# Kernel optimization log

Measured on AMD Instinct MI355X. Metric: run time of the kernel, lower is better.

Reference implementation:

```python
import jax, jax.numpy as jnp
import numpy as np

B, S, D, H = 16, 784, 768, 12
DH = D // H  # 64


def rotate_half(x):
    # (x1, x2, x3, x4) -> (-x2, x1, -x4, x3), interleaved
    x_even = x[..., ::2]
    x_odd = x[..., 1::2]
    return jnp.stack((-x_odd, x_even), axis=-1).reshape(x.shape)


def setup_inputs() -> dict:
    key = jax.random.key(0)
    ks = jax.random.split(key, 12)
    s = 0.02
    return {
        "hidden_states": jax.random.normal(ks[0], (B, S, D), jnp.float32),
        "rotary_pos_emb": jax.random.uniform(ks[1], (B, S, DH), jnp.float32) * 6.28,
        "wq": jax.random.normal(ks[2], (D, D), jnp.float32) * s,
        "bq": jax.random.normal(ks[3], (D,), jnp.float32) * s,
        "wk": jax.random.normal(ks[4], (D, D), jnp.float32) * s,
        "bk": jax.random.normal(ks[5], (D,), jnp.float32) * s,
        "wv": jax.random.normal(ks[6], (D, D), jnp.float32) * s,
        "bv": jax.random.normal(ks[7], (D,), jnp.float32) * s,
        "wo": jax.random.normal(ks[8], (D, D), jnp.float32) * s,
        "bo": jax.random.normal(ks[9], (D,), jnp.float32) * s,
    }


def reference(hidden_states, rotary_pos_emb, wq, bq, wk, bk, wv, bv, wo, bo):
    scale = DH ** -0.5
    # Linear: x @ W^T + b; reshape to [B, H, S, DH]
    def proj(w, b):
        y = jnp.einsum("bsd,ed->bse", hidden_states, w) + b
        return y.reshape(B, S, H, DH).transpose(0, 2, 1, 3)

    q = proj(wq, bq)
    k = proj(wk, bk)
    v = proj(wv, bv)

    # RoPE: freqs [B, S, DH] -> [B, 1, S, DH] broadcast over heads
    cos = jnp.cos(rotary_pos_emb)[:, None, :, :]
    sin = jnp.sin(rotary_pos_emb)[:, None, :, :]
    q = q * cos + rotate_half(q) * sin
    k = k * cos + rotate_half(k) * sin

    attn = jnp.einsum("bhqd,bhkd->bhqk", q, k) * scale
    attn = jax.nn.softmax(attn, axis=-1)
    out = jnp.einsum("bhqk,bhkd->bhqd", attn, v)
    out = out.transpose(0, 2, 1, 3).reshape(B, S, D)
    out = jnp.einsum("bsd,ed->bse", out, wo) + bo
    return out
```

## Files before the change

kernel.cpp:

```cpp
#include <hip/hip_runtime.h>
#include <cstdint>
#include <cstddef>

constexpr int kB  = 16;
constexpr int kS  = 784;
constexpr int kD  = 768;
constexpr int kH  = 12;
constexpr int kM  = kB * kS;
constexpr int kSP = 832;

typedef __attribute__((ext_vector_type(8))) short bf16x8;
typedef __attribute__((ext_vector_type(4))) float floatx4;

__device__ __forceinline__ unsigned short f2bf(float x) {
    union { float f; unsigned int u; } v; v.f = x;
    unsigned int r = v.u + 0x7fffu + ((v.u >> 16) & 1u);
    return (unsigned short)(r >> 16);
}
__device__ __forceinline__ float bf2f(unsigned short h) {
    union { unsigned int u; float f; } v; v.u = ((unsigned int)h) << 16;
    return v.f;
}

__device__ __forceinline__ void gload_lds16(const void* g, void* l) {
    __builtin_amdgcn_global_load_lds(
        (const __attribute__((address_space(1))) void*)g,
        (__attribute__((address_space(3))) void*)l,
        16, 0, 0);
}

constexpr int kHsF4   = (kM * kD) / 4;
constexpr int kWF4    = (kD * kD) / 4;
constexpr int kPreTot = kHsF4 + 4 * kWF4 + (kM * 64) / 4;

__global__ __launch_bounds__(256)
void convert_pre(const float* __restrict__ hs, const float* __restrict__ rot,
                 const float* __restrict__ wq, const float* __restrict__ wk,
                 const float* __restrict__ wv, const float* __restrict__ wo,
                 const float* __restrict__ bq, const float* __restrict__ bk,
                 const float* __restrict__ bv,
                 unsigned short* __restrict__ hsB, unsigned short* __restrict__ wB,
                 unsigned int* __restrict__ csT, float* __restrict__ biasC)
{
    const int i = blockIdx.x * 256 + threadIdx.x;
    if (i < kHsF4) {
        float4 v = ((const float4*)hs)[i];
        ushort4 o = { f2bf(v.x), f2bf(v.y), f2bf(v.z), f2bf(v.w) };
        ((ushort4*)hsB)[i] = o;
    } else if (i < kHsF4 + 4 * kWF4) {
        const int j = i - kHsF4;
        const int w = j / kWF4, jj = j - w * kWF4;
        const float* src = (w == 0) ? wq : (w == 1) ? wk : (w == 2) ? wv : wo;
        float4 v = ((const float4*)src)[jj];
        ushort4 o = { f2bf(v.x), f2bf(v.y), f2bf(v.z), f2bf(v.w) };
        ((ushort4*)(wB + (size_t)w * (kD * kD)))[jj] = o;
    } else if (i < kPreTot) {
        const int j = i - kHsF4 - 4 * kWF4;
        float4 v = ((const float4*)rot)[j];
        float a[4] = { v.x, v.y, v.z, v.w };
        #pragma unroll
        for (int e = 0; e < 4; ++e) {
            float s, c;
            __sincosf(a[e], &s, &c);
            csT[j * 4 + e] = (unsigned)f2bf(c) | ((unsigned)f2bf(s) << 16);
        }
    } else {
        const int j = i - kPreTot;
        if (j < 3 * kD)
            biasC[j] = (j < kD) ? bq[j] : (j < 2 * kD) ? bk[j - kD] : bv[j - 2 * kD];
    }
}

enum { MODE_QKV = 0, MODE_OUT = 1 };

template<int MODE>
__global__ __launch_bounds__(256, 2)
void gemm_k(const unsigned short* __restrict__ A, const unsigned short* __restrict__ W,
            const float* __restrict__ bias, const unsigned int* __restrict__ csT,
            unsigned short* __restrict__ Qp, unsigned short* __restrict__ Kp,
            unsigned short* __restrict__ Vtp, float* __restrict__ Op)
{
    constexpr int BN  = (MODE == MODE_QKV) ? 256 : 128;
    constexpr int NTL = (MODE == MODE_QKV) ? 9 : 6;
    constexpr int NTC = BN / 32;
    constexpr int WJ  = BN / 64;

    __shared__ unsigned short As[2][4096];
    __shared__ unsigned short Ws[2][BN * 32];

    const int lin   = blockIdx.x;
    const int group = lin / (8 * NTL);
    const int rem   = lin - group * (8 * NTL);
    const int base_m = group * 8;
    int m_tile, n_tile;
    if (base_m + 8 <= 98) { m_tile = base_m + (rem & 7); n_tile = rem >> 3; }
    else                  { m_tile = base_m + (rem & 1); n_tile = rem >> 1; }
    const int m0 = m_tile * 128;
    const int n0 = n_tile * BN;

    const int tid  = threadIdx.x;
    const int wave = tid >> 6;
    const int lane = tid & 63;
    const int quad = lane >> 4;
    const int l16  = lane & 15;
    const int wm = wave >> 1, wn = wave & 1;

    floatx4 acc[4][NTC];
    #pragma unroll
    for (int mt = 0; mt < 4; ++mt)
        #pragma unroll
        for (int nt = 0; nt < NTC; ++nt)
            acc[mt][nt] = {0.f, 0.f, 0.f, 0.f};

    const int sidx0 = wave * 128 + lane;
    const int srow0 = sidx0 >> 2, sseg0 = (sidx0 & 3) ^ ((srow0 >> 1) & 3);
    const int sidx1 = sidx0 + 64;
    const int srow1 = sidx1 >> 2, sseg1 = (sidx1 & 3) ^ ((srow1 >> 1) & 3);
    int wrow[WJ], wseg[WJ];
    #pragma unroll
    for (int j = 0; j < WJ; ++j) {
        const int cid = wave * BN + j * 64 + lane;
        wrow[j] = cid >> 2;
        wseg[j] = (cid & 3) ^ ((wrow[j] >> 1) & 3);
    }

    gload_lds16(A + (size_t)(m0 + srow0) * kD + sseg0 * 8, &As[0][wave * 1024]);
    gload_lds16(A + (size_t)(m0 + srow1) * kD + sseg1 * 8, &As[0][wave * 1024 + 512]);
    #pragma unroll
    for (int j = 0; j < WJ; ++j)
        gload_lds16(W + (size_t)(n0 + wrow[j]) * kD + wseg[j] * 8,
                    &Ws[0][(wave * BN + j * 64) * 8]);

    for (int ks = 0; ks < 24; ++ks) {
        __syncthreads();
        if (ks < 23) {
            const int nb = (ks + 1) & 1;
            const int k0 = (ks + 1) * 32;
            gload_lds16(A + (size_t)(m0 + srow0) * kD + k0 + sseg0 * 8, &As[nb][wave * 1024]);
            gload_lds16(A + (size_t)(m0 + srow1) * kD + k0 + sseg1 * 8, &As[nb][wave * 1024 + 512]);
            #pragma unroll
            for (int j = 0; j < WJ; ++j)
                gload_lds16(W + (size_t)(n0 + wrow[j]) * kD + k0 + wseg[j] * 8,
                            &Ws[nb][(wave * BN + j * 64) * 8]);
        }
        const unsigned short* as_ = As[ks & 1];
        const unsigned short* ws_ = Ws[ks & 1];

        bf16x8 af[4], bw[NTC];
        #pragma unroll
        for (int mt = 0; mt < 4; ++mt) {
            const int row = wm * 64 + mt * 16 + l16;
            const int slot = quad ^ ((row >> 1) & 3);
            af[mt] = *(const bf16x8*)&as_[row * 32 + slot * 8];
        }
        #pragma unroll
        for (int nt = 0; nt < NTC; ++nt) {
            const int row = wn * (BN / 2) + nt * 16 + l16;
            const int slot = quad ^ ((row >> 1) & 3);
            bw[nt] = *(const bf16x8*)&ws_[row * 32 + slot * 8];
        }
        #pragma unroll
        for (int mt = 0; mt < 4; ++mt)
            #pragma unroll
            for (int nt = 0; nt < NTC; ++nt)
                acc[mt][nt] = __builtin_amdgcn_mfma_f32_16x16x32_bf16(
                    af[mt], bw[nt], acc[mt][nt], 0, 0, 0);
    }

    if constexpr (MODE == MODE_OUT) {
        #pragma unroll
        for (int nt = 0; nt < NTC; ++nt) {
            const int n = n0 + wn * (BN / 2) + nt * 16 + l16;
            const float bv = bias[n];
            #pragma unroll
            for (int mt = 0; mt < 4; ++mt)
                #pragma unroll
                for (int r = 0; r < 4; ++r) {
                    const int m = m0 + wm * 64 + mt * 16 + quad * 4 + r;
                    Op[(size_t)m * kD + n] = acc[mt][nt][r] + bv;
                }
        }
    } else {
        const int proj = n_tile / 3;
        if (proj < 2) {
            unsigned short* dst = proj ? Kp : Qp;
            const float scale = proj ? 1.0f : 0.125f;
            #pragma unroll
            for (int nt = 0; nt < NTC; ++nt) {
                const int n = n0 + wn * (BN / 2) + nt * 16 + l16;
                const float bv = bias[n];
                const int col = n - proj * kD;
                const int dh = col & 63;
                const int odd = l16 & 1;
                #pragma unroll
                for (int mt = 0; mt < 4; ++mt)
                    #pragma unroll
                    for (int r = 0; r < 4; ++r) {
                        const int m = m0 + wm * 64 + mt * 16 + quad * 4 + r;
                        const float val = acc[mt][nt][r] + bv;
                        const float px = __shfl_xor(val, 1);
                        const unsigned u = csT[(size_t)m * 64 + dh];
                        const float c = bf2f((unsigned short)(u & 0xffffu));
                        const float s = bf2f((unsigned short)(u >> 16));
                        const float out = odd ? (val * c + px * s) : (val * c - px * s);
                        dst[(size_t)m * kD + col] = f2bf(out * scale);
                    }
            }
        } else {
            #pragma unroll
            for (int nt = 0; nt < NTC; ++nt) {
                const int n = n0 + wn * (BN / 2) + nt * 16 + l16;
                const float bv = bias[n];
                const int col = n - 2 * kD;
                const int h = col >> 6, dh = col & 63;
                #pragma unroll
                for (int mt = 0; mt < 4; ++mt) {
                    const int m_r0 = m0 + wm * 64 + mt * 16 + quad * 4;
                    const int b = m_r0 / kS;
                    const int s = m_r0 - b * kS;
                    ushort4 pk;
                    pk.x = f2bf(acc[mt][nt][0] + bv);
                    pk.y = f2bf(acc[mt][nt][1] + bv);
                    pk.z = f2bf(acc[mt][nt][2] + bv);
                    pk.w = f2bf(acc[mt][nt][3] + bv);
                    *(ushort4*)(Vtp + (size_t)((b * kH + h) * 64 + dh) * kSP + s) = pk;
                }
            }
        }
    }
}

__global__ __launch_bounds__(256)
void flash_attn(const unsigned short* __restrict__ Qg,
                const unsigned short* __restrict__ Kg,
                const unsigned short* __restrict__ Vtg,
                unsigned short* __restrict__ Og)
{
    __shared__ unsigned short KV[2][8192];
    __shared__ unsigned short Ps[4][32 * 68];

    const int lin   = blockIdx.x;
    const int group = lin / 56;
    const int rem   = lin - group * 56;
    const int bh = group * 8 + (rem & 7);
    const int qt = rem >> 3;
    const int b = bh / kH, h = bh - b * kH;
    const int tid = threadIdx.x, wave = tid >> 6, lane = tid & 63;
    const int quad = lane >> 4, l16 = lane & 15;
    const int q0 = qt * 128;
    const size_t rowBase = (size_t)(b * kS) * kD + h * 64;

    #pragma unroll
    for (int j = 0; j < 4; ++j) {
        const int idx = (wave * 4 + j) * 64 + lane;
        const int row = idx >> 3, slot = idx & 7, seg = slot ^ (row & 7);
        gload_lds16(Qg + rowBase + (size_t)(q0 + row) * kD + seg * 8,
                    &KV[0][(wave * 4 + j) * 512]);
    }
    __syncthreads();
    bf16x8 aq[2][2];
    #pragma unroll
    for (int mt = 0; mt < 2; ++mt)
        #pragma unroll
        for (int ch = 0; ch < 2; ++ch) {
            const int row = wave * 32 + mt * 16 + l16;
            const int slot = (ch * 4 + quad) ^ (row & 7);
            aq[mt][ch] = *(const bf16x8*)&KV[0][row * 64 + slot * 8];
        }
    __syncthreads();

    const int cidx0 = wave * 128 + lane;
    const int crow0 = cidx0 >> 3, cseg0 = (cidx0 & 7) ^ (crow0 & 7);
    const int cidx1 = cidx0 + 64;
    const int crow1 = cidx1 >> 3, cseg1 = (cidx1 & 7) ^ (crow1 & 7);

    {
        gload_lds16(Kg + rowBase + (size_t)(crow0)*kD + cseg0 * 8, &KV[0][wave * 1024]);
        gload_lds16(Vtg + (size_t)(bh * 64 + crow0) * kSP + cseg0 * 8, &KV[0][4096 + wave * 1024]);
        gload_lds16(Kg + rowBase + (size_t)(crow1)*kD + cseg1 * 8, &KV[0][wave * 1024 + 512]);
        gload_lds16(Vtg + (size_t)(bh * 64 + crow1) * kSP + cseg1 * 8, &KV[0][4096 + wave * 1024 + 512]);
    }

    floatx4 oacc[2][4];
    #pragma unroll
    for (int mt = 0; mt < 2; ++mt)
        #pragma unroll
        for (int nt = 0; nt < 4; ++nt)
            oacc[mt][nt] = {0.f, 0.f, 0.f, 0.f};
    float lrow[2][4];
    #pragma unroll
    for (int mt = 0; mt < 2; ++mt)
        #pragma unroll
        for (int r = 0; r < 4; ++r) lrow[mt][r] = 0.f;

    for (int kt = 0; kt < 13; ++kt) {
        __syncthreads();
        if (kt < 12) {
            const int nb = (kt + 1) & 1;
            const int kr = (kt + 1) * 64;
            gload_lds16(Kg + rowBase + (size_t)(kr + crow0) * kD + cseg0 * 8,
                        &KV[nb][wave * 1024]);
            gload_lds16(Vtg + (size_t)(bh * 64 + crow0) * kSP + kr + cseg0 * 8,
                        &KV[nb][4096 + wave * 1024]);
            gload_lds16(Kg + rowBase + (size_t)(kr + crow1) * kD + cseg1 * 8,
                        &KV[nb][wave * 1024 + 512]);
            gload_lds16(Vtg + (size_t)(bh * 64 + crow1) * kSP + kr + cseg1 * 8,
                        &KV[nb][4096 + wave * 1024 + 512]);
        }
        const unsigned short* Ks = &KV[kt & 1][0];
        const unsigned short* Vs = &KV[kt & 1][4096];

        bf16x8 bk[4][2];
        #pragma unroll
        for (int nt = 0; nt < 4; ++nt)
            #pragma unroll
            for (int ch = 0; ch < 2; ++ch) {
                const int row = nt * 16 + l16;
                const int slot = (ch * 4 + quad) ^ (row & 7);
                bk[nt][ch] = *(const bf16x8*)&Ks[row * 64 + slot * 8];
            }

        floatx4 sc[2][4];
        #pragma unroll
        for (int mt = 0; mt < 2; ++mt)
            #pragma unroll
            for (int nt = 0; nt < 4; ++nt) {
                sc[mt][nt] = {0.f, 0.f, 0.f, 0.f};
                sc[mt][nt] = __builtin_amdgcn_mfma_f32_16x16x32_bf16(
                    aq[mt][0], bk[nt][0], sc[mt][nt], 0, 0, 0);
                sc[mt][nt] = __builtin_amdgcn_mfma_f32_16x16x32_bf16(
                    aq[mt][1], bk[nt][1], sc[mt][nt], 0, 0, 0);
            }

        if (kt == 12) {
            #pragma unroll
            for (int mt = 0; mt < 2; ++mt)
                #pragma unroll
                for (int nt = 1; nt < 4; ++nt)
                    #pragma unroll
                    for (int r = 0; r < 4; ++r) sc[mt][nt][r] = -1e30f;
        }

        #pragma unroll
        for (int mt = 0; mt < 2; ++mt)
            #pragma unroll
            for (int nt = 0; nt < 4; ++nt)
                #pragma unroll
                for (int r = 0; r < 4; ++r) {
                    const float p = __expf(sc[mt][nt][r]);
                    union { float f; unsigned u; } pu; pu.f = p;
                    union { unsigned u; float f; } pt; pt.u = pu.u & 0xFFFF0000u;
                    lrow[mt][r] += pt.f;
                    Ps[wave][(mt * 16 + quad * 4 + r) * 68 + nt * 16 + l16] =
                        (unsigned short)(pu.u >> 16);
                }

        bf16x8 ap[2][2];
        #pragma unroll
        for (int mt = 0; mt < 2; ++mt)
            #pragma unroll
            for (int ks = 0; ks < 2; ++ks)
                ap[mt][ks] = *(const bf16x8*)&Ps[wave][(mt * 16 + l16) * 68 + ks * 32 + quad * 8];

        #pragma unroll
        for (int ks = 0; ks < 2; ++ks)
            #pragma unroll
            for (int nt = 0; nt < 4; ++nt) {
                const int row = nt * 16 + l16;
                const int slot = (ks * 4 + quad) ^ (row & 7);
                const bf16x8 bv = *(const bf16x8*)&Vs[row * 64 + slot * 8];
                #pragma unroll
                for (int mt = 0; mt < 2; ++mt)
                    oacc[mt][nt] = __builtin_amdgcn_mfma_f32_16x16x32_bf16(
                        ap[mt][ks], bv, oacc[mt][nt], 0, 0, 0);
            }
    }

    #pragma unroll
    for (int mt = 0; mt < 2; ++mt)
        #pragma unroll
        for (int r = 0; r < 4; ++r) {
            float l = lrow[mt][r];
            #pragma unroll
            for (int off = 1; off < 16; off <<= 1) l += __shfl_xor(l, off);
            lrow[mt][r] = 1.0f / l;
        }

    #pragma unroll
    for (int mt = 0; mt < 2; ++mt)
        #pragma unroll
        for (int r = 0; r < 4; ++r) {
            const int srow = q0 + wave * 32 + mt * 16 + quad * 4 + r;
            if (srow < kS) {
                const float inv = lrow[mt][r];
                #pragma unroll
                for (int nt = 0; nt < 4; ++nt)
                    Og[rowBase + (size_t)srow * kD + nt * 16 + l16] =
                        f2bf(oacc[mt][nt][r] * inv);
            }
        }
}

extern "C" void kernel_launch(void* const* d_in, const int* in_sizes, int n_in,
                              void* d_out, int out_size, void* d_ws, size_t ws_size,
                              hipStream_t stream)
{
    (void)in_sizes; (void)n_in; (void)out_size; (void)ws_size;
    const float* hs  = (const float*)d_in[0];
    const float* rot = (const float*)d_in[1];
    const float* wq  = (const float*)d_in[2];
    const float* bq  = (const float*)d_in[3];
    const float* wk  = (const float*)d_in[4];
    const float* bk  = (const float*)d_in[5];
    const float* wv  = (const float*)d_in[6];
    const float* bv  = (const float*)d_in[7];
    const float* wo  = (const float*)d_in[8];
    const float* bo  = (const float*)d_in[9];

    char* ws = (char*)d_ws;
    unsigned short* hsB  = (unsigned short*)ws;
    unsigned short* wB   = (unsigned short*)(ws + 19267584);
    unsigned int*   csT  = (unsigned int*)(ws + 23986176);
    float*          biasC= (float*)(ws + 27197440);
    unsigned short* Q    = (unsigned short*)(ws + 27206656);
    unsigned short* K    = (unsigned short*)(ws + 46474240);
    unsigned short* Vt   = (unsigned short*)(ws + 65741824);
    unsigned short* O    = hsB;

    const dim3 blk(256);

    convert_pre<<<dim3(12505), blk, 0, stream>>>(hs, rot, wq, wk, wv, wo, bq, bk, bv,
                                                 hsB, wB, csT, biasC);
    gemm_k<MODE_QKV><<<dim3(882), blk, 0, stream>>>(
        hsB, wB, biasC, csT, Q, K, Vt, nullptr);
    flash_attn<<<dim3(7 * 192), blk, 0, stream>>>(Q, K, Vt, O);
    gemm_k<MODE_OUT><<<dim3(588), blk, 0, stream>>>(
        O, wB + 3 * kD * kD, bo, nullptr, nullptr, nullptr, nullptr, (float*)d_out);
}
```

Measured before the change: 275.9 us.

## Triple-buffer GEMM LDS staging with explicit vmcnt waits; raise MFMA wave priority

The QKV and output-projection GEMM loop moves from double to triple buffering of LDS tiles. It prefetches two k-steps ahead and uses explicit s_waitcnt vmcnt counts plus raw s_barrier instead of __syncthreads, so global loads overlap more compute. The attention kernel also wraps its MFMA sections in s_setprio(1) so matrix work is favoured across waves. The cost is more LDS per block, which may reduce occupancy, and the hand-written vmcnt counts must match the exact number of loads issued per stage.

```diff
diff --git a/kernel.cpp b/kernel.cpp
--- a/kernel.cpp
+++ b/kernel.cpp
@@ -85,8 +85,8 @@
     constexpr int NTC = BN / 32;
     constexpr int WJ  = BN / 64;
 
-    __shared__ unsigned short As[2][4096];
-    __shared__ unsigned short Ws[2][BN * 32];
+    __shared__ unsigned short As[3][4096];
+    __shared__ unsigned short Ws[3][BN * 32];
 
     const int lin   = blockIdx.x;
     const int group = lin / (8 * NTL);
@@ -124,27 +124,37 @@
         wseg[j] = (cid & 3) ^ ((wrow[j] >> 1) & 3);
     }
 
-    gload_lds16(A + (size_t)(m0 + srow0) * kD + sseg0 * 8, &As[0][wave * 1024]);
-    gload_lds16(A + (size_t)(m0 + srow1) * kD + sseg1 * 8, &As[0][wave * 1024 + 512]);
-    #pragma unroll
-    for (int j = 0; j < WJ; ++j)
-        gload_lds16(W + (size_t)(n0 + wrow[j]) * kD + wseg[j] * 8,
-                    &Ws[0][(wave * BN + j * 64) * 8]);
-
+    auto stage = [&](int ks, int buf) {
+        const int k0 = ks * 32;
+        gload_lds16(A + (size_t)(m0 + srow0) * kD + k0 + sseg0 * 8, &As[buf][wave * 1024]);
+        gload_lds16(A + (size_t)(m0 + srow1) * kD + k0 + sseg1 * 8, &As[buf][wave * 1024 + 512]);
+        #pragma unroll
+        for (int j = 0; j < WJ; ++j)
+            gload_lds16(W + (size_t)(n0 + wrow[j]) * kD + k0 + wseg[j] * 8,
+                        &Ws[buf][(wave * BN + j * 64) * 8]);
+    };
+
+    stage(0, 0);
+    stage(1, 1);
+
+    int cur = 0;
+    int pre = 2;
     for (int ks = 0; ks < 24; ++ks) {
-        __syncthreads();
-        if (ks < 23) {
-            const int nb = (ks + 1) & 1;
-            const int k0 = (ks + 1) * 32;
-            gload_lds16(A + (size_t)(m0 + srow0) * kD + k0 + sseg0 * 8, &As[nb][wave * 1024]);
-            gload_lds16(A + (size_t)(m0 + srow1) * kD + k0 + sseg1 * 8, &As[nb][wave * 1024 + 512]);
-            #pragma unroll
-            for (int j = 0; j < WJ; ++j)
-                gload_lds16(W + (size_t)(n0 + wrow[j]) * kD + k0 + wseg[j] * 8,
-                            &Ws[nb][(wave * BN + j * 64) * 8]);
-        }
-        const unsigned short* as_ = As[ks & 1];
-        const unsigned short* ws_ = Ws[ks & 1];
+        asm volatile("s_barrier" ::: "memory");
+        if (ks < 22) stage(ks + 2, pre);
+        if (ks < 22) {
+            if constexpr (MODE == MODE_QKV) asm volatile("s_waitcnt vmcnt(12)" ::: "memory");
+            else                            asm volatile("s_waitcnt vmcnt(8)"  ::: "memory");
+        } else if (ks == 22) {
+            if constexpr (MODE == MODE_QKV) asm volatile("s_waitcnt vmcnt(6)" ::: "memory");
+            else                            asm volatile("s_waitcnt vmcnt(4)" ::: "memory");
+        } else {
+            asm volatile("s_waitcnt vmcnt(0)" ::: "memory");
+        }
+        asm volatile("s_barrier" ::: "memory");
+
+        const unsigned short* as_ = As[cur];
+        const unsigned short* ws_ = Ws[cur];
 
         bf16x8 af[4], bw[NTC];
         #pragma unroll
@@ -165,6 +175,9 @@
             for (int nt = 0; nt < NTC; ++nt)
                 acc[mt][nt] = __builtin_amdgcn_mfma_f32_16x16x32_bf16(
                     af[mt], bw[nt], acc[mt][nt], 0, 0, 0);
+
+        cur = (cur == 2) ? 0 : cur + 1;
+        pre = (pre == 2) ? 0 : pre + 1;
     }
 
     if constexpr (MODE == MODE_OUT) {
@@ -321,6 +334,7 @@
             }
 
         floatx4 sc[2][4];
+        __builtin_amdgcn_s_setprio(1);
         #pragma unroll
         for (int mt = 0; mt < 2; ++mt)
             #pragma unroll
@@ -331,6 +345,7 @@
                 sc[mt][nt] = __builtin_amdgcn_mfma_f32_16x16x32_bf16(
                     aq[mt][1], bk[nt][1], sc[mt][nt], 0, 0, 0);
             }
+        __builtin_amdgcn_s_setprio(0);
 
         if (kt == 12) {
             #pragma unroll
@@ -362,6 +377,7 @@
             for (int ks = 0; ks < 2; ++ks)
                 ap[mt][ks] = *(const bf16x8*)&Ps[wave][(mt * 16 + l16) * 68 + ks * 32 + quad * 8];
 
+        __builtin_amdgcn_s_setprio(1);
         #pragma unroll
         for (int ks = 0; ks < 2; ++ks)
             #pragma unroll
@@ -374,6 +390,7 @@
                     oacc[mt][nt] = __builtin_amdgcn_mfma_f32_16x16x32_bf16(
                         ap[mt][ks], bv, oacc[mt][nt], 0, 0, 0);
             }
+        __builtin_amdgcn_s_setprio(0);
     }
 
     #pragma unroll
```

New measurement: 265.1 us. 1.04x faster.

## Rewrite GEMMs as 256x256-tile 8-wave kernels with ping-pong pipelined LDS staging

Applied to the files above, without the earlier changes.

Replaces the 128xBN GEMM with a 512-thread kernel computing 256x256 tiles, 64-wide K steps in two halves, double-buffered 128KB LDS, explicit s_waitcnt/barrier scheduling and s_setprio around MFMA bursts. The goal is more data reuse per tile and better overlap of global-to-LDS loads with matrix math. Flash attention also gets setprio around its MFMA sections. Larger tiles reduce block count (441 and 147 blocks), which risks wave quantization and lower occupancy on 256 CUs, and the hand-placed waitcnts are fragile.

```diff
diff --git a/kernel.cpp b/kernel.cpp
--- a/kernel.cpp
+++ b/kernel.cpp
@@ -73,111 +73,130 @@
 
 enum { MODE_QKV = 0, MODE_OUT = 1 };
 
+#define BARR  __builtin_amdgcn_s_barrier()
+#define LGK0  asm volatile("s_waitcnt lgkmcnt(0)" ::: "memory")
+#define VM4   asm volatile("s_waitcnt vmcnt(4)" ::: "memory")
+#define VM0   asm volatile("s_waitcnt vmcnt(0)" ::: "memory")
+#define PRIO1 __builtin_amdgcn_s_setprio(1)
+#define PRIO0 __builtin_amdgcn_s_setprio(0)
+
+#define LDA4(KS, RB, MQ) do{ \
+  afr[0]=*(const bf16x8*)(rdA##KS+(RB)+((MQ)+0)*4096); \
+  afr[1]=*(const bf16x8*)(rdA##KS+(RB)+((MQ)+1)*4096); \
+  afr[2]=*(const bf16x8*)(rdA##KS+(RB)+((MQ)+2)*4096); \
+  afr[3]=*(const bf16x8*)(rdA##KS+(RB)+((MQ)+3)*4096); }while(0)
+
+#define LDB4(KS, RB) do{ \
+  bfr[0]=*(const bf16x8*)(rdB##KS+(RB)); \
+  bfr[1]=*(const bf16x8*)(rdB##KS+(RB)+8192); \
+  bfr[2]=*(const bf16x8*)(rdB##KS+(RB)+16384); \
+  bfr[3]=*(const bf16x8*)(rdB##KS+(RB)+24576); }while(0)
+
+#define MFMA16(MQ) do{ _Pragma("unroll") for(int nt=0;nt<4;++nt){ \
+  acc[(MQ)  ][nt]=__builtin_amdgcn_mfma_f32_16x16x32_bf16(afr[0],bfr[nt],acc[(MQ)  ][nt],0,0,0); \
+  acc[(MQ)+1][nt]=__builtin_amdgcn_mfma_f32_16x16x32_bf16(afr[1],bfr[nt],acc[(MQ)+1][nt],0,0,0); \
+  acc[(MQ)+2][nt]=__builtin_amdgcn_mfma_f32_16x16x32_bf16(afr[2],bfr[nt],acc[(MQ)+2][nt],0,0,0); \
+  acc[(MQ)+3][nt]=__builtin_amdgcn_mfma_f32_16x16x32_bf16(afr[3],bfr[nt],acc[(MQ)+3][nt],0,0,0); \
+}}while(0)
+
+#define KTILE(RB, SB, KT) do{ \
+   LDA4(0, RB, 0); LDB4(0, RB); \
+    if ((KT) <= 10) { stA(1, (KT)+1, SB); stB(1, (KT)+1, SB); } \
+    BARR; LGK0; PRIO1; MFMA16(0); PRIO0; BARR; \
+   LDA4(0, RB, 4); \
+    BARR; LGK0; PRIO1; MFMA16(4); PRIO0; BARR; \
+   LDA4(1, RB, 0); LDB4(1, RB); \
+    BARR; LGK0; PRIO1; MFMA16(0); PRIO0; BARR; \
+   LDA4(1, RB, 4); \
+    if ((KT) <= 9) { stA(0, (KT)+2, RB); stB(0, (KT)+2, RB); VM4; } \
+    else if ((KT) == 10) { VM0; } \
+    BARR; LGK0; PRIO1; MFMA16(4); PRIO0; BARR; \
+}while(0)
+
 template<int MODE>
-__global__ __launch_bounds__(256, 2)
-void gemm_k(const unsigned short* __restrict__ A, const unsigned short* __restrict__ W,
-            const float* __restrict__ bias, const unsigned int* __restrict__ csT,
-            unsigned short* __restrict__ Qp, unsigned short* __restrict__ Kp,
-            unsigned short* __restrict__ Vtp, float* __restrict__ Op)
+__global__ __launch_bounds__(512, 2)
+void gemm8(const unsigned short* __restrict__ A, const unsigned short* __restrict__ W,
+           const float* __restrict__ bias, const unsigned int* __restrict__ csT,
+           unsigned short* __restrict__ Qp, unsigned short* __restrict__ Kp,
+           unsigned short* __restrict__ Vtp, float* __restrict__ Op)
 {
-    constexpr int BN  = (MODE == MODE_QKV) ? 256 : 128;
-    constexpr int NTL = (MODE == MODE_QKV) ? 9 : 6;
-    constexpr int NTC = BN / 32;
-    constexpr int WJ  = BN / 64;
-
-    __shared__ unsigned short As[2][4096];
-    __shared__ unsigned short Ws[2][BN * 32];
+    constexpr int NTL = (MODE == MODE_QKV) ? 9 : 3;
+
+    __shared__ unsigned short SM[65536];
 
     const int lin   = blockIdx.x;
     const int group = lin / (8 * NTL);
     const int rem   = lin - group * (8 * NTL);
-    const int base_m = group * 8;
     int m_tile, n_tile;
-    if (base_m + 8 <= 98) { m_tile = base_m + (rem & 7); n_tile = rem >> 3; }
-    else                  { m_tile = base_m + (rem & 1); n_tile = rem >> 1; }
-    const int m0 = m_tile * 128;
-    const int n0 = n_tile * BN;
+    if (group < 6) { m_tile = group * 8 + (rem & 7); n_tile = rem >> 3; }
+    else           { m_tile = 48; n_tile = rem; }
+    const int m0 = m_tile * 256;
+    const int n0 = n_tile * 256;
 
     const int tid  = threadIdx.x;
     const int wave = tid >> 6;
     const int lane = tid & 63;
-    const int quad = lane >> 4;
-    const int l16  = lane & 15;
-    const int wm = wave >> 1, wn = wave & 1;
-
-    floatx4 acc[4][NTC];
-    #pragma unroll
-    for (int mt = 0; mt < 4; ++mt)
-        #pragma unroll
-        for (int nt = 0; nt < NTC; ++nt)
-            acc[mt][nt] = {0.f, 0.f, 0.f, 0.f};
-
-    const int sidx0 = wave * 128 + lane;
-    const int srow0 = sidx0 >> 2, sseg0 = (sidx0 & 3) ^ ((srow0 >> 1) & 3);
-    const int sidx1 = sidx0 + 64;
-    const int srow1 = sidx1 >> 2, sseg1 = (sidx1 & 3) ^ ((srow1 >> 1) & 3);
-    int wrow[WJ], wseg[WJ];
-    #pragma unroll
-    for (int j = 0; j < WJ; ++j) {
-        const int cid = wave * BN + j * 64 + lane;
-        wrow[j] = cid >> 2;
-        wseg[j] = (cid & 3) ^ ((wrow[j] >> 1) & 3);
-    }
-
-    gload_lds16(A + (size_t)(m0 + srow0) * kD + sseg0 * 8, &As[0][wave * 1024]);
-    gload_lds16(A + (size_t)(m0 + srow1) * kD + sseg1 * 8, &As[0][wave * 1024 + 512]);
-    #pragma unroll
-    for (int j = 0; j < WJ; ++j)
-        gload_lds16(W + (size_t)(n0 + wrow[j]) * kD + wseg[j] * 8,
-                    &Ws[0][(wave * BN + j * 64) * 8]);
-
-    for (int ks = 0; ks < 24; ++ks) {
-        __syncthreads();
-        if (ks < 23) {
-            const int nb = (ks + 1) & 1;
-            const int k0 = (ks + 1) * 32;
-            gload_lds16(A + (size_t)(m0 + srow0) * kD + k0 + sseg0 * 8, &As[nb][wave * 1024]);
-            gload_lds16(A + (size_t)(m0 + srow1) * kD + k0 + sseg1 * 8, &As[nb][wave * 1024 + 512]);
-            #pragma unroll
-            for (int j = 0; j < WJ; ++j)
-                gload_lds16(W + (size_t)(n0 + wrow[j]) * kD + k0 + wseg[j] * 8,
-                            &Ws[nb][(wave * BN + j * 64) * 8]);
-        }
-        const unsigned short* as_ = As[ks & 1];
-        const unsigned short* ws_ = Ws[ks & 1];
-
-        bf16x8 af[4], bw[NTC];
-        #pragma unroll
-        for (int mt = 0; mt < 4; ++mt) {
-            const int row = wm * 64 + mt * 16 + l16;
-            const int slot = quad ^ ((row >> 1) & 3);
-            af[mt] = *(const bf16x8*)&as_[row * 32 + slot * 8];
-        }
-        #pragma unroll
-        for (int nt = 0; nt < NTC; ++nt) {
-            const int row = wn * (BN / 2) + nt * 16 + l16;
-            const int slot = quad ^ ((row >> 1) & 3);
-            bw[nt] = *(const bf16x8*)&ws_[row * 32 + slot * 8];
-        }
-        #pragma unroll
-        for (int mt = 0; mt < 4; ++mt)
-            #pragma unroll
-            for (int nt = 0; nt < NTC; ++nt)
-                acc[mt][nt] = __builtin_amdgcn_mfma_f32_16x16x32_bf16(
-                    af[mt], bw[nt], acc[mt][nt], 0, 0, 0);
+    const int quad = lane >> 4, l16 = lane & 15;
+    const int wm = wave & 1;
+    const int wn = wave >> 1;
+
+    const int l8  = lane >> 3;
+    const int sc  = (lane & 7) ^ l8;
+    const unsigned short* gA0 = A + (size_t)(m0 + wave * 16 + l8) * kD + sc * 8;
+    const unsigned short* gA1 = gA0 + (size_t)8 * kD;
+    const unsigned short* gB0 = W + (size_t)(n0 + wave * 16 + l8) * kD + sc * 8;
+    const unsigned short* gB1 = gB0 + (size_t)8 * kD;
+    char* smc = (char*)SM;
+
+    auto stA = [&](int h, int kt, int bufoff) {
+        const int off = h * 98304 + kt * 64;
+        gload_lds16(gA0 + off, smc + bufoff + h * 16384 + wave * 2048);
+        gload_lds16(gA1 + off, smc + bufoff + h * 16384 + wave * 2048 + 1024);
+    };
+    auto stB = [&](int h, int kt, int bufoff) {
+        const int off = h * 98304 + kt * 64;
+        gload_lds16(gB0 + off, smc + 65536 + bufoff + h * 16384 + wave * 2048);
+        gload_lds16(gB1 + off, smc + 65536 + bufoff + h * 16384 + wave * 2048 + 1024);
+    };
+
+    const int swz0 = ((quad    ) ^ (l16 & 7)) * 16;
+    const int swz1 = ((quad + 4) ^ (l16 & 7)) * 16;
+    const char* rdA0 = (const char*)SM + (wm * 16 + l16) * 128 + swz0;
+    const char* rdA1 = (const char*)SM + (wm * 16 + l16) * 128 + swz1;
+    const char* rdB0 = (const char*)SM + 65536 + (wn * 16 + l16) * 128 + swz0;
+    const char* rdB1 = (const char*)SM + 65536 + (wn * 16 + l16) * 128 + swz1;
+
+    floatx4 acc[8][4];
+    #pragma unroll
+    for (int m = 0; m < 8; ++m)
+        #pragma unroll
+        for (int nt = 0; nt < 4; ++nt)
+            acc[m][nt] = {0.f, 0.f, 0.f, 0.f};
+    bf16x8 afr[4], bfr[4];
+
+    stA(0, 0, 0);      stB(0, 0, 0);
+    stA(1, 0, 0);      stB(1, 0, 0);
+    stA(0, 1, 32768);  stB(0, 1, 32768);
+    VM4;
+    BARR;
+
+    #pragma unroll
+    for (int ktp = 0; ktp < 6; ++ktp) {
+        KTILE(0,     32768, ktp * 2);
+        KTILE(32768, 0,     ktp * 2 + 1);
     }
 
     if constexpr (MODE == MODE_OUT) {
         #pragma unroll
-        for (int nt = 0; nt < NTC; ++nt) {
-            const int n = n0 + wn * (BN / 2) + nt * 16 + l16;
+        for (int nt = 0; nt < 4; ++nt) {
+            const int n = n0 + nt * 64 + wn * 16 + l16;
             const float bv = bias[n];
             #pragma unroll
-            for (int mt = 0; mt < 4; ++mt)
+            for (int m = 0; m < 8; ++m)
                 #pragma unroll
                 for (int r = 0; r < 4; ++r) {
-                    const int m = m0 + wm * 64 + mt * 16 + quad * 4 + r;
-                    Op[(size_t)m * kD + n] = acc[mt][nt][r] + bv;
+                    const int mm = m0 + m * 32 + wm * 16 + quad * 4 + r;
+                    Op[(size_t)mm * kD + n] = acc[m][nt][r] + bv;
                 }
         }
     } else {
@@ -186,43 +205,43 @@
             unsigned short* dst = proj ? Kp : Qp;
             const float scale = proj ? 1.0f : 0.125f;
             #pragma unroll
-            for (int nt = 0; nt < NTC; ++nt) {
-                const int n = n0 + wn * (BN / 2) + nt * 16 + l16;
+            for (int nt = 0; nt < 4; ++nt) {
+                const int n = n0 + nt * 64 + wn * 16 + l16;
                 const float bv = bias[n];
                 const int col = n - proj * kD;
                 const int dh = col & 63;
                 const int odd = l16 & 1;
                 #pragma unroll
-                for (int mt = 0; mt < 4; ++mt)
+                for (int m = 0; m < 8; ++m)
                     #pragma unroll
                     for (int r = 0; r < 4; ++r) {
-                        const int m = m0 + wm * 64 + mt * 16 + quad * 4 + r;
-                        const float val = acc[mt][nt][r] + bv;
+                        const int mm = m0 + m * 32 + wm * 16 + quad * 4 + r;
+                        const float val = acc[m][nt][r] + bv;
                         const float px = __shfl_xor(val, 1);
-                        const unsigned u = csT[(size_t)m * 64 + dh];
+                        const unsigned u = csT[(size_t)mm * 64 + dh];
                         const float c = bf2f((unsigned short)(u & 0xffffu));
                         const float s = bf2f((unsigned short)(u >> 16));
                         const float out = odd ? (val * c + px * s) : (val * c - px * s);
-                        dst[(size_t)m * kD + col] = f2bf(out * scale);
+                        dst[(size_t)mm * kD + col] = f2bf(out * scale);
                     }
             }
         } else {
             #pragma unroll
-            for (int nt = 0; nt < NTC; ++nt) {
-                const int n = n0 + wn * (BN / 2) + nt * 16 + l16;
+            for (int nt = 0; nt < 4; ++nt) {
+                const int n = n0 + nt * 64 + wn * 16 + l16;
                 const float bv = bias[n];
                 const int col = n - 2 * kD;
                 const int h = col >> 6, dh = col & 63;
                 #pragma unroll
-                for (int mt = 0; mt < 4; ++mt) {
-                    const int m_r0 = m0 + wm * 64 + mt * 16 + quad * 4;
+                for (int m = 0; m < 8; ++m) {
+                    const int m_r0 = m0 + m * 32 + wm * 16 + quad * 4;
                     const int b = m_r0 / kS;
                     const int s = m_r0 - b * kS;
                     ushort4 pk;
-                    pk.x = f2bf(acc[mt][nt][0] + bv);
-                    pk.y = f2bf(acc[mt][nt][1] + bv);
-                    pk.z = f2bf(acc[mt][nt][2] + bv);
-                    pk.w = f2bf(acc[mt][nt][3] + bv);
+                    pk.x = f2bf(acc[m][nt][0] + bv);
+                    pk.y = f2bf(acc[m][nt][1] + bv);
+                    pk.z = f2bf(acc[m][nt][2] + bv);
+                    pk.w = f2bf(acc[m][nt][3] + bv);
                     *(ushort4*)(Vtp + (size_t)((b * kH + h) * 64 + dh) * kSP + s) = pk;
                 }
             }
@@ -321,6 +340,7 @@
             }
 
         floatx4 sc[2][4];
+        __builtin_amdgcn_s_setprio(1);
         #pragma unroll
         for (int mt = 0; mt < 2; ++mt)
             #pragma unroll
@@ -331,6 +351,7 @@
                 sc[mt][nt] = __builtin_amdgcn_mfma_f32_16x16x32_bf16(
                     aq[mt][1], bk[nt][1], sc[mt][nt], 0, 0, 0);
             }
+        __builtin_amdgcn_s_setprio(0);
 
         if (kt == 12) {
             #pragma unroll
@@ -362,6 +383,7 @@
             for (int ks = 0; ks < 2; ++ks)
                 ap[mt][ks] = *(const bf16x8*)&Ps[wave][(mt * 16 + l16) * 68 + ks * 32 + quad * 8];
 
+        __builtin_amdgcn_s_setprio(1);
         #pragma unroll
         for (int ks = 0; ks < 2; ++ks)
             #pragma unroll
@@ -374,6 +396,7 @@
                     oacc[mt][nt] = __builtin_amdgcn_mfma_f32_16x16x32_bf16(
                         ap[mt][ks], bv, oacc[mt][nt], 0, 0, 0);
             }
+        __builtin_amdgcn_s_setprio(0);
     }
 
     #pragma unroll
@@ -427,13 +450,11 @@
     unsigned short* Vt   = (unsigned short*)(ws + 65741824);
     unsigned short* O    = hsB;
 
-    const dim3 blk(256);
-
-    convert_pre<<<dim3(12505), blk, 0, stream>>>(hs, rot, wq, wk, wv, wo, bq, bk, bv,
-                                                 hsB, wB, csT, biasC);
-    gemm_k<MODE_QKV><<<dim3(882), blk, 0, stream>>>(
+    convert_pre<<<dim3(12505), dim3(256), 0, stream>>>(hs, rot, wq, wk, wv, wo, bq, bk, bv,
+                                                       hsB, wB, csT, biasC);
+    gemm8<MODE_QKV><<<dim3(441), dim3(512), 0, stream>>>(
         hsB, wB, biasC, csT, Q, K, Vt, nullptr);
-    flash_attn<<<dim3(7 * 192), blk, 0, stream>>>(Q, K, Vt, O);
-    gemm_k<MODE_OUT><<<dim3(588), blk, 0, stream>>>(
+    flash_attn<<<dim3(7 * 192), dim3(256), 0, stream>>>(Q, K, Vt, O);
+    gemm8<MODE_OUT><<<dim3(147), dim3(512), 0, stream>>>(
         O, wB + 3 * kD * kD, bo, nullptr, nullptr, nullptr, nullptr, (float*)d_out);
 }
```

After: 257.1 us. 6.8% less time.
